# Kernel optimization log

Measured on AMD Instinct MI355X. Metric: run time of the kernel, lower is better.

Reference implementation:

```python
import jax, jax.numpy as jnp
import numpy as np

T, D, H, E, K = 8192, 2048, 7168, 8, 2


def setup_inputs() -> dict:
    key = jax.random.key(0)
    ks = jax.random.split(key, 5)
    s = 0.02
    return {
        "x": jax.random.normal(ks[0], (T, D), jnp.float32),
        "gate_w": jax.random.normal(ks[1], (E, D), jnp.float32) * s,
        "w1": jax.random.normal(ks[2], (E, H, D), jnp.float32) * s,
        "w2": jax.random.normal(ks[3], (E, H, D), jnp.float32) * s,
        "w3": jax.random.normal(ks[4], (E, H, D), jnp.float32) * s,
    }


def reference(x, gate_w, w1, w2, w3):
    # gate logits [T, E]
    logits = x @ gate_w.T
    vals, idx = jax.lax.top_k(logits, K)                      # [T, K]
    w = jax.nn.softmax(vals.astype(jnp.float32), axis=-1).astype(x.dtype)
    # per-token routing weight for each expert (0 if not selected) [T, E]
    tok = jnp.arange(x.shape[0])
    expert_w = jnp.zeros((x.shape[0], E), x.dtype).at[tok[:, None], idx].add(w)

    # scan over experts: dense SwiGLU per expert, weighted accumulate
    def body(acc, ws):
        w1e, w2e, w3e, we = ws  # [H,D],[H,D],[H,D],[T]
        y = (jax.nn.silu(x @ w1e.T) * (x @ w3e.T)) @ w2e      # [T, D]
        return acc + we[:, None] * y, None

    res, _ = jax.lax.scan(body, jnp.zeros_like(x), (w1, w2, w3, expert_w.T))
    return res
```

## Files before the change

kernel.cpp:

```cpp
#include <hip/hip_runtime.h>

#define TT   8192
#define DDIM 2048
#define HDIM 7168
#define NEXP 8
#define MT   32
#define NT1  (HDIM / 128)
#define NT2  (DDIM / 256)
#define NTILE_MAX 72

typedef __attribute__((ext_vector_type(8))) short bf16x8;
typedef __attribute__((ext_vector_type(8))) short short8v;
typedef __attribute__((ext_vector_type(4))) short short4v;
typedef __attribute__((ext_vector_type(4))) float f32x4;

__device__ __forceinline__ unsigned short f2bf(float f) {
  unsigned int u = __builtin_bit_cast(unsigned int, f);
  u += 0x7fffu + ((u >> 16) & 1u);
  return (unsigned short)(u >> 16);
}

__device__ __forceinline__ float bf2f(unsigned short h) {
  unsigned int u = ((unsigned int)h) << 16;
  return __builtin_bit_cast(float, u);
}

__device__ __forceinline__ void gload_lds16(const void* gp, void* lp) {
  __builtin_amdgcn_global_load_lds((__attribute__((address_space(1))) void*)gp,
                                   (__attribute__((address_space(3))) void*)lp,
                                   16, 0, 0);
}

__device__ __forceinline__ void mfma16(f32x4& c, bf16x8 a, bf16x8 b) {
  c = __builtin_amdgcn_mfma_f32_16x16x32_bf16(a, b, c, 0, 0, 0);
}

__device__ __forceinline__ void wg_barrier() {
  asm volatile("" ::: "memory");
  __builtin_amdgcn_s_barrier();
  asm volatile("" ::: "memory");
}

#define PH(H, BA, BB, RDB, STG, SRCP, SOFF, VM)                              \
  do {                                                                       \
    if (RDB) {                                                               \
      _Pragma("unroll")                                                      \
      for (int n = 0; n < 4; ++n)                                            \
        bfr[n] = *(const bf16x8*)(smem + (BB) + rB + n * 1024);              \
    }                                                                        \
    _Pragma("unroll")                                                        \
    for (int m = 0; m < 4; ++m)                                              \
      af[m] = *(const bf16x8*)(smem + (BA) + rA + ((H) + m) * 1024);         \
    if ((STG) >= 0) {                                                        \
      gload_lds16(SRCP[0] + (SOFF), smem + (STG) + wid * 2048);              \
      gload_lds16(SRCP[1] + (SOFF), smem + (STG) + wid * 2048 + 1024);       \
    }                                                                        \
    wg_barrier();                                                            \
    __builtin_amdgcn_s_setprio(1);                                           \
    _Pragma("unroll")                                                        \
    for (int n = 0; n < 4; ++n) {                                            \
      _Pragma("unroll")                                                      \
      for (int m = 0; m < 4; ++m)                                            \
        mfma16(acc[(H) + m][n], af[m], bfr[n]);                              \
    }                                                                        \
    __builtin_amdgcn_s_setprio(0);                                           \
    if ((VM) == 6) asm volatile("s_waitcnt vmcnt(6)" ::: "memory");          \
    if ((VM) == 0) asm volatile("s_waitcnt vmcnt(0)" ::: "memory");          \
    wg_barrier();                                                            \
  } while (0)

#define ITER_FULL(kb)                                                        \
  PH(0, 0,     32768,  1, 81920,  asrc, (kb) + 192, -1);                     \
  PH(4, 0,     32768,  0, 32768,  bsrc, (kb) + 256, -1);                     \
  PH(0, 16384, 49152,  1, 0,      asrc, (kb) + 256, -1);                     \
  PH(4, 16384, 49152,  0, 49152,  bsrc, (kb) + 320,  6);                     \
  PH(0, 65536, 98304,  1, 16384,  asrc, (kb) + 320, -1);                     \
  PH(4, 65536, 98304,  0, 98304,  bsrc, (kb) + 384, -1);                     \
  PH(0, 81920, 114688, 1, 65536,  asrc, (kb) + 384, -1);                     \
  PH(4, 81920, 114688, 0, 114688, bsrc, (kb) + 448,  6);

#define ITER_LAST(kb)                                                        \
  PH(0, 0,     32768,  1, 81920,  asrc, (kb) + 192, -1);                     \
  PH(4, 0,     32768,  0, -1,     asrc, 0,          -1);                     \
  PH(0, 16384, 49152,  1, -1,     asrc, 0,          -1);                     \
  PH(4, 16384, 49152,  0, -1,     asrc, 0,           0);                     \
  PH(0, 65536, 98304,  1, -1,     asrc, 0,          -1);                     \
  PH(4, 65536, 98304,  0, -1,     asrc, 0,          -1);                     \
  PH(0, 81920, 114688, 1, -1,     asrc, 0,          -1);                     \
  PH(4, 81920, 114688, 0, -1,     asrc, 0,          -1);

#define PROLOGUE()                                                           \
  do {                                                                       \
    gload_lds16(asrc[0] + 0,   smem + 0      + wid * 2048);                  \
    gload_lds16(asrc[1] + 0,   smem + 0      + wid * 2048 + 1024);           \
    gload_lds16(bsrc[0] + 0,   smem + 32768  + wid * 2048);                  \
    gload_lds16(bsrc[1] + 0,   smem + 32768  + wid * 2048 + 1024);           \
    gload_lds16(asrc[0] + 64,  smem + 16384  + wid * 2048);                  \
    gload_lds16(asrc[1] + 64,  smem + 16384  + wid * 2048 + 1024);           \
    gload_lds16(bsrc[0] + 64,  smem + 49152  + wid * 2048);                  \
    gload_lds16(bsrc[1] + 64,  smem + 49152  + wid * 2048 + 1024);           \
    gload_lds16(bsrc[0] + 128, smem + 98304  + wid * 2048);                  \
    gload_lds16(bsrc[1] + 128, smem + 98304  + wid * 2048 + 1024);           \
    gload_lds16(asrc[0] + 128, smem + 65536  + wid * 2048);                  \
    gload_lds16(asrc[1] + 128, smem + 65536  + wid * 2048 + 1024);           \
    gload_lds16(bsrc[0] + 192, smem + 114688 + wid * 2048);                  \
    gload_lds16(bsrc[1] + 192, smem + 114688 + wid * 2048 + 1024);           \
    asm volatile("s_waitcnt vmcnt(6)" ::: "memory");                         \
    wg_barrier();                                                            \
  } while (0)

__global__ __launch_bounds__(256) void cvt_bf16_kernel(const float* __restrict__ src,
                                                       unsigned short* __restrict__ dst,
                                                       long n8) {
  long i = (long)blockIdx.x * 256 + threadIdx.x;
  long stride = (long)gridDim.x * 256;
  for (; i < n8; i += stride) {
    float4 a = ((const float4*)src)[i * 2];
    float4 b = ((const float4*)src)[i * 2 + 1];
    short8v s;
    s[0] = (short)f2bf(a.x); s[1] = (short)f2bf(a.y);
    s[2] = (short)f2bf(a.z); s[3] = (short)f2bf(a.w);
    s[4] = (short)f2bf(b.x); s[5] = (short)f2bf(b.y);
    s[6] = (short)f2bf(b.z); s[7] = (short)f2bf(b.w);
    ((short8v*)dst)[i] = s;
  }
}

__global__ __launch_bounds__(256) void gate_kernel(const float* __restrict__ x,
                                                   const float* __restrict__ gw,
                                                   int* __restrict__ route_e,
                                                   float* __restrict__ route_w,
                                                   int* __restrict__ counts) {
  int t = blockIdx.x;
  int tid = threadIdx.x;
  const float* xr = x + (size_t)t * DDIM;
  float p[NEXP];
#pragma unroll
  for (int e = 0; e < NEXP; ++e) p[e] = 0.f;
#pragma unroll
  for (int c = 0; c < DDIM / (256 * 4); ++c) {
    int d = (c * 256 + tid) * 4;
    float4 xv = *(const float4*)(xr + d);
#pragma unroll
    for (int e = 0; e < NEXP; ++e) {
      float4 wv = *(const float4*)(gw + (size_t)e * DDIM + d);
      p[e] += xv.x * wv.x + xv.y * wv.y + xv.z * wv.z + xv.w * wv.w;
    }
  }
  __shared__ float red[NEXP][4];
  int lane = tid & 63, wid = tid >> 6;
#pragma unroll
  for (int e = 0; e < NEXP; ++e) {
    float v = p[e];
    for (int o = 32; o > 0; o >>= 1) v += __shfl_down(v, o);
    if (lane == 0) red[e][wid] = v;
  }
  __syncthreads();
  if (tid == 0) {
    float lg[NEXP];
#pragma unroll
    for (int e = 0; e < NEXP; ++e) lg[e] = red[e][0] + red[e][1] + red[e][2] + red[e][3];
    int i0 = 0;
#pragma unroll
    for (int e = 1; e < NEXP; ++e) if (lg[e] > lg[i0]) i0 = e;
    int i1 = -1;
#pragma unroll
    for (int e = 0; e < NEXP; ++e) {
      if (e == i0) continue;
      if (i1 < 0 || lg[e] > lg[i1]) i1 = e;
    }
    float w0 = 1.f / (1.f + __expf(lg[i1] - lg[i0]));
    float w1 = 1.f - w0;
    route_e[t * 2 + 0] = i0;  route_e[t * 2 + 1] = i1;
    route_w[t * 2 + 0] = w0;  route_w[t * 2 + 1] = w1;
    atomicAdd(&counts[i0], 1);
    atomicAdd(&counts[i1], 1);
  }
}

__global__ void scan_kernel(const int* __restrict__ counts, int* __restrict__ offsets,
                            int* __restrict__ cursor, int* __restrict__ tmap) {
  if (threadIdx.x == 0 && blockIdx.x == 0) {
    int o = 0, idx = 0;
    for (int e = 0; e < NEXP; ++e) {
      offsets[e] = o; cursor[e] = o;
      int c = counts[e]; o += c;
      for (int t = 0; t * 256 < c && idx < NTILE_MAX; ++t) tmap[1 + idx++] = (e << 16) | t;
    }
    tmap[0] = idx;
  }
}

__global__ __launch_bounds__(256) void scatter_kernel(const int* __restrict__ route_e,
                                                      const float* __restrict__ route_w,
                                                      int* __restrict__ cursor,
                                                      int* __restrict__ tok_list,
                                                      float* __restrict__ tok_w,
                                                      int* __restrict__ slot_of) {
  int t = blockIdx.x * 256 + threadIdx.x;
  if (t >= TT) return;
#pragma unroll
  for (int s = 0; s < 2; ++s) {
    int e = route_e[t * 2 + s];
    int p = atomicAdd(&cursor[e], 1);
    tok_list[p] = t;
    tok_w[p] = route_w[t * 2 + s];
    slot_of[t * 2 + s] = p;
  }
}

__global__ __launch_bounds__(256) void transpose_w2_kernel(const float* __restrict__ w2,
                                                           unsigned short* __restrict__ w2t,
                                                           int expert_fixed) {
  int e = expert_fixed >= 0 ? expert_fixed : (int)blockIdx.z;
  const float* src = w2 + (size_t)e * HDIM * DDIM;
  unsigned short* dst = w2t + (expert_fixed >= 0 ? (size_t)0 : (size_t)e * DDIM * HDIM);
  int h0 = blockIdx.x * 64, d0 = blockIdx.y * 64;
  __shared__ __align__(8) unsigned short tile[64 * 66];
  int tid = threadIdx.x;
  int hr = tid >> 2;
#pragma unroll
  for (int j = 0; j < 4; ++j) {
    int f4 = (tid & 3) + j * 4;
    float4 v = *(const float4*)(src + (size_t)(h0 + hr) * DDIM + d0 + f4 * 4);
    unsigned int lo = (unsigned int)f2bf(v.x) | ((unsigned int)f2bf(v.y) << 16);
    unsigned int hi = (unsigned int)f2bf(v.z) | ((unsigned int)f2bf(v.w) << 16);
    char* bp = (char*)tile + hr * 132 + f4 * 8;
    *(unsigned int*)bp = lo;
    *(unsigned int*)(bp + 4) = hi;
  }
  __syncthreads();
  int dr = tid >> 2;
  int hbase = (tid & 3) * 16;
  unsigned short vals[16];
#pragma unroll
  for (int i = 0; i < 16; ++i)
    vals[i] = *(unsigned short*)((char*)tile + (hbase + i) * 132 + dr * 2);
  unsigned short* op = dst + (size_t)(d0 + dr) * HDIM + h0 + hbase;
  short8v s0, s1;
#pragma unroll
  for (int i = 0; i < 8; ++i) { s0[i] = (short)vals[i]; s1[i] = (short)vals[i + 8]; }
  *(short8v*)(op) = s0;
  *(short8v*)(op + 8) = s1;
}

__global__ __launch_bounds__(256) void reduce_kernel(const unsigned short* __restrict__ ybuf,
                                                     const int* __restrict__ slot_of,
                                                     const float* __restrict__ route_w,
                                                     float* __restrict__ out) {
  int t = blockIdx.x;
  int d = threadIdx.x * 8;
  int s0 = slot_of[t * 2 + 0], s1 = slot_of[t * 2 + 1];
  float w0 = route_w[t * 2 + 0], w1 = route_w[t * 2 + 1];
  bf16x8 y0 = *(const bf16x8*)(ybuf + (size_t)s0 * DDIM + d);
  bf16x8 y1 = *(const bf16x8*)(ybuf + (size_t)s1 * DDIM + d);
  float4 o0, o1;
  o0.x = w0 * bf2f((unsigned short)y0[0]) + w1 * bf2f((unsigned short)y1[0]);
  o0.y = w0 * bf2f((unsigned short)y0[1]) + w1 * bf2f((unsigned short)y1[1]);
  o0.z = w0 * bf2f((unsigned short)y0[2]) + w1 * bf2f((unsigned short)y1[2]);
  o0.w = w0 * bf2f((unsigned short)y0[3]) + w1 * bf2f((unsigned short)y1[3]);
  o1.x = w0 * bf2f((unsigned short)y0[4]) + w1 * bf2f((unsigned short)y1[4]);
  o1.y = w0 * bf2f((unsigned short)y0[5]) + w1 * bf2f((unsigned short)y1[5]);
  o1.z = w0 * bf2f((unsigned short)y0[6]) + w1 * bf2f((unsigned short)y1[6]);
  o1.w = w0 * bf2f((unsigned short)y0[7]) + w1 * bf2f((unsigned short)y1[7]);
  float* op = out + (size_t)t * DDIM + d;
  *(float4*)op = o0;
  *(float4*)(op + 4) = o1;
}

__global__ __launch_bounds__(512, 2) void gemm1_kernel(
    const unsigned short* __restrict__ xbf, const unsigned short* __restrict__ w1b,
    const unsigned short* __restrict__ w3b, const int* __restrict__ tok_list,
    const int* __restrict__ counts, const int* __restrict__ offsets,
    const int* __restrict__ tmap,
    unsigned short* __restrict__ g, int expert_fixed) {
  __shared__ __align__(16) char smem[133120];
  constexpr int NI = DDIM / 128;

  int nwg = gridDim.x;
  int orig = blockIdx.x;
  int wg = (orig & 7) * (nwg >> 3) + (orig >> 3);
  int e, mbase, nt;
  if (expert_fixed >= 0) {
    e = expert_fixed;
    mbase = (wg & (MT - 1)) * 256;
    nt = (wg >> 5) % NT1;
  } else {
    int tl = wg % NTILE_MAX;
    nt = wg / NTILE_MAX;
    if (tl >= tmap[0]) return;
    int pk = tmap[1 + tl];
    e = pk >> 16;
    mbase = (pk & 0xffff) * 256;
  }
  int cnt = counts[e];
  if (mbase >= cnt) return;
  int off = offsets[e];
  int gshift = expert_fixed >= 0 ? 0 : off;
  int rows = cnt - mbase; if (rows > 256) rows = 256;

  const unsigned short* w1e = expert_fixed >= 0 ? w1b : w1b + (size_t)e * HDIM * DDIM;
  const unsigned short* w3e = expert_fixed >= 0 ? w3b : w3b + (size_t)e * HDIM * DDIM;

  int tid = threadIdx.x, lane = tid & 63, wid = tid >> 6;
  int wr = wid >> 2, wc = wid & 3;

  int r16 = lane >> 2;
  int csrc = (lane & 3) ^ ((lane >> 3) & 3);
  const char* asrc[2]; const char* bsrc[2];
#pragma unroll
  for (int j = 0; j < 2; ++j) {
    int r = wid * 32 + j * 16 + r16;
    int m = mbase + r; if (m > cnt - 1) m = cnt - 1;
    int tok = tok_list[off + m];
    asrc[j] = (const char*)xbf + (size_t)tok * (DDIM * 2) + csrc * 16;
    const char* base = (r < 128)
        ? (const char*)w1e + (size_t)(nt * 128 + r) * (DDIM * 2)
        : (const char*)w3e + (size_t)(nt * 128 + r - 128) * (DDIM * 2);
    bsrc[j] = base + csrc * 16;
  }
  int rA = (wr * 128 + (lane & 15)) * 64 + (((lane >> 4) ^ ((lane >> 1) & 3)) * 16);
  int rB = (wc * 64  + (lane & 15)) * 64 + (((lane >> 4) ^ ((lane >> 1) & 3)) * 16);

  f32x4 zv = {0.f, 0.f, 0.f, 0.f};
  f32x4 acc[8][4];
#pragma unroll
  for (int m = 0; m < 8; ++m)
#pragma unroll
    for (int n = 0; n < 4; ++n) acc[m][n] = zv;
  bf16x8 af[4], bfr[4];

  PROLOGUE();
#pragma unroll 1
  for (int i = 0; i < NI - 1; ++i) {
    size_t kb = (size_t)i * 256;
    ITER_FULL(kb);
  }
  {
    size_t kb = (size_t)(NI - 1) * 256;
    ITER_LAST(kb);
  }

  float* hb = (float*)smem;
  if (wc < 2) {
#pragma unroll
    for (int m = 0; m < 8; ++m)
#pragma unroll
      for (int q = 0; q < 4; ++q) {
        int row = wr * 128 + m * 16 + (lane >> 4) * 4 + q;
        int col = wc * 64 + (lane & 15);
#pragma unroll
        for (int n = 0; n < 4; ++n)
          hb[row * 130 + col + n * 16] = acc[m][n][q];
      }
  }
  asm volatile("s_waitcnt lgkmcnt(0)" ::: "memory");
  wg_barrier();
  if (wc >= 2) {
#pragma unroll
    for (int m = 0; m < 8; ++m)
#pragma unroll
      for (int q = 0; q < 4; ++q) {
        int row = wr * 128 + m * 16 + (lane >> 4) * 4 + q;
        if (row >= rows) continue;
        size_t grow = (size_t)(mbase + row + gshift);
        int colbase = (wc - 2) * 64 + (lane & 15);
        unsigned short* gp = g + grow * HDIM + nt * 128 + colbase;
#pragma unroll
        for (int n = 0; n < 4; ++n) {
          float h1 = hb[row * 130 + colbase + n * 16];
          float h3 = acc[m][n][q];
          float gv = (h1 / (1.f + __expf(-h1))) * h3;
          gp[n * 16] = f2bf(gv);
        }
      }
  }
}

__global__ __launch_bounds__(512, 2) void gemm2_kernel(
    const unsigned short* __restrict__ g, const unsigned short* __restrict__ w2t,
    const int* __restrict__ tok_list, const float* __restrict__ tok_w,
    const int* __restrict__ counts, const int* __restrict__ offsets,
    const int* __restrict__ tmap,
    unsigned short* __restrict__ ybuf, float* __restrict__ out, int expert_fixed) {
  __shared__ __align__(16) char smem[131072];
  constexpr int NI = HDIM / 128;

  int nwg = gridDim.x;
  int orig = blockIdx.x;
  int wg = (orig & 7) * (nwg >> 3) + (orig >> 3);
  int e, mbase, nt;
  if (expert_fixed >= 0) {
    e = expert_fixed;
    nt = wg % NT2;
    mbase = (wg / NT2) * 256;
  } else {
    int tl = wg / NT2;
    nt = wg % NT2;
    if (tl >= tmap[0]) return;
    int pk = tmap[1 + tl];
    e = pk >> 16;
    mbase = (pk & 0xffff) * 256;
  }
  int cnt = counts[e];
  if (mbase >= cnt) return;
  int off = offsets[e];
  int gshift = expert_fixed >= 0 ? 0 : off;
  int nbase = nt * 256;
  int rows = cnt - mbase; if (rows > 256) rows = 256;
  const unsigned short* w2te = w2t + (expert_fixed >= 0 ? (size_t)0 : (size_t)e * DDIM * HDIM);

  int tid = threadIdx.x, lane = tid & 63, wid = tid >> 6;
  int wr = wid >> 2, wc = wid & 3;

  int r16 = lane >> 2;
  int csrc = (lane & 3) ^ ((lane >> 3) & 3);
  const char* asrc[2]; const char* bsrc[2];
#pragma unroll
  for (int j = 0; j < 2; ++j) {
    int r = wid * 32 + j * 16 + r16;
    int m = mbase + r; if (m > cnt - 1) m = cnt - 1;
    asrc[j] = (const char*)g + (size_t)(m + gshift) * (HDIM * 2) + csrc * 16;
    bsrc[j] = (const char*)w2te + (size_t)(nbase + r) * (HDIM * 2) + csrc * 16;
  }
  int rA = (wr * 128 + (lane & 15)) * 64 + (((lane >> 4) ^ ((lane >> 1) & 3)) * 16);
  int rB = (wc * 64  + (lane & 15)) * 64 + (((lane >> 4) ^ ((lane >> 1) & 3)) * 16);

  f32x4 zv = {0.f, 0.f, 0.f, 0.f};
  f32x4 acc[8][4];
#pragma unroll
  for (int m = 0; m < 8; ++m)
#pragma unroll
    for (int n = 0; n < 4; ++n) acc[m][n] = zv;
  bf16x8 af[4], bfr[4];

  PROLOGUE();
#pragma unroll 1
  for (int i = 0; i < NI - 1; ++i) {
    size_t kb = (size_t)i * 256;
    ITER_FULL(kb);
  }
  {
    size_t kb = (size_t)(NI - 1) * 256;
    ITER_LAST(kb);
  }

  if (ybuf) {
#pragma unroll
    for (int m = 0; m < 8; ++m)
#pragma unroll
      for (int q = 0; q < 4; ++q) {
        int row = wr * 128 + m * 16 + (lane >> 4) * 4 + q;
        if (row >= rows) continue;
        size_t slot = (size_t)(off + mbase + row);
        unsigned short* yp = ybuf + slot * DDIM + nbase + wc * 64 + (lane & 15);
#pragma unroll
        for (int n = 0; n < 4; ++n)
          yp[n * 16] = f2bf(acc[m][n][q]);
      }
  } else {
#pragma unroll
    for (int m = 0; m < 8; ++m)
#pragma unroll
      for (int q = 0; q < 4; ++q) {
        int row = wr * 128 + m * 16 + (lane >> 4) * 4 + q;
        if (row >= rows) continue;
        int mi = mbase + row;
        int tok = tok_list[off + mi];
        float wt = tok_w[off + mi];
        float* op = out + (size_t)tok * DDIM + nbase + wc * 64 + (lane & 15);
#pragma unroll
        for (int n = 0; n < 4; ++n)
          atomicAdd(op + n * 16, acc[m][n][q] * wt);
      }
  }
}

extern "C" void kernel_launch(void* const* d_in, const int* in_sizes, int n_in,
                              void* d_out, int out_size, void* d_ws, size_t ws_size,
                              hipStream_t stream) {
  const float* x      = (const float*)d_in[0];
  const float* gate_w = (const float*)d_in[1];
  const float* w1     = (const float*)d_in[2];
  const float* w2     = (const float*)d_in[3];
  const float* w3     = (const float*)d_in[4];
  float* out = (float*)d_out;
  char* ws = (char*)d_ws;

  size_t o = 0;
  int* counts  = (int*)(ws + o);
  int* offsets = counts + 8;
  int* cursor  = counts + 16;
  int* tmap    = counts + 24;
  o += 1024;
  int*   route_e = (int*)(ws + o);   o += (size_t)TT * 2 * 4;
  float* route_w = (float*)(ws + o); o += (size_t)TT * 2 * 4;
  int*   tok_list = (int*)(ws + o);  o += (size_t)TT * 2 * 4;
  float* tok_w = (float*)(ws + o);   o += (size_t)TT * 2 * 4;
  int*   slot_of = (int*)(ws + o);   o += (size_t)TT * 2 * 4;
  unsigned short* xbf = (unsigned short*)(ws + o); o += (size_t)TT * DDIM * 2;
  size_t fixed = o;

  const size_t WSZ = (size_t)HDIM * DDIM;
  const size_t wbf_full = (size_t)NEXP * WSZ * 2;
  const size_t gfull = (size_t)TT * 2 * HDIM * 2;

  hipMemsetAsync(counts, 0, 8 * sizeof(int), stream);
  cvt_bf16_kernel<<<4096, 256, 0, stream>>>(x, xbf, (long)TT * DDIM / 8);
  gate_kernel<<<TT, 256, 0, stream>>>(x, gate_w, route_e, route_w, counts);
  scan_kernel<<<1, 64, 0, stream>>>(counts, offsets, cursor, tmap);
  scatter_kernel<<<(TT + 255) / 256, 256, 0, stream>>>(route_e, route_w, cursor,
                                                       tok_list, tok_w, slot_of);

  if (ws_size >= fixed + 3 * wbf_full + gfull) {
    unsigned short* w1b = (unsigned short*)(ws + fixed);
    unsigned short* w3b = w1b + NEXP * WSZ;
    unsigned short* w2t = w3b + NEXP * WSZ;
    unsigned short* gbuf = w2t + NEXP * WSZ;
    unsigned short* ybuf = w1b;
    cvt_bf16_kernel<<<8192, 256, 0, stream>>>(w1, w1b, (long)(NEXP * WSZ / 8));
    cvt_bf16_kernel<<<8192, 256, 0, stream>>>(w3, w3b, (long)(NEXP * WSZ / 8));
    transpose_w2_kernel<<<dim3(HDIM / 64, DDIM / 64, NEXP), 256, 0, stream>>>(w2, w2t, -1);
    gemm1_kernel<<<NTILE_MAX * NT1, 512, 0, stream>>>(
        xbf, w1b, w3b, tok_list, counts, offsets, tmap, gbuf, -1);
    gemm2_kernel<<<NTILE_MAX * NT2, 512, 0, stream>>>(
        gbuf, w2t, tok_list, tok_w, counts, offsets, tmap, ybuf, out, -1);
    reduce_kernel<<<TT, 256, 0, stream>>>(ybuf, slot_of, route_w, out);
  } else {
    unsigned short* w1b = (unsigned short*)(ws + fixed);
    unsigned short* w3b = w1b + WSZ;
    unsigned short* w2t = w3b + WSZ;
    unsigned short* gbuf = w2t + WSZ;
    hipMemsetAsync(out, 0, (size_t)TT * DDIM * sizeof(float), stream);
    for (int e = 0; e < NEXP; ++e) {
      cvt_bf16_kernel<<<4096, 256, 0, stream>>>(w1 + (size_t)e * WSZ, w1b, (long)(WSZ / 8));
      cvt_bf16_kernel<<<4096, 256, 0, stream>>>(w3 + (size_t)e * WSZ, w3b, (long)(WSZ / 8));
      transpose_w2_kernel<<<dim3(HDIM / 64, DDIM / 64, 1), 256, 0, stream>>>(w2, w2t, e);
      gemm1_kernel<<<MT * NT1, 512, 0, stream>>>(
          xbf, w1b, w3b, tok_list, counts, offsets, tmap, gbuf, e);
      gemm2_kernel<<<MT * NT2, 512, 0, stream>>>(
          gbuf, w2t, tok_list, tok_w, counts, offsets, tmap, (unsigned short*)0, out, e);
    }
  }
}
```

Measured before the change: 2.254 ms.

## Double-buffer B fragments and prefetch next B tile from LDS during MFMA

Replaces the compiler-generated LDS reads with inline ds_read_b128 and keeps two B-fragment register sets. The next phase's B fragments are read while the current phase's MFMAs run, with explicit lgkmcnt waits and sched_barriers added. The aim is to hide LDS read latency behind matrix math in both GEMM kernels. In exchange it uses more VGPRs, and the manual waitcnt bookkeeping could race if the counts are wrong.

```diff
diff --git a/kernel.cpp b/kernel.cpp
--- a/kernel.cpp
+++ b/kernel.cpp
@@ -13,6 +13,7 @@
 typedef __attribute__((ext_vector_type(8))) short short8v;
 typedef __attribute__((ext_vector_type(4))) short short4v;
 typedef __attribute__((ext_vector_type(4))) float f32x4;
+typedef const __attribute__((address_space(3))) char* lds_ptr;
 
 __device__ __forceinline__ unsigned short f2bf(float f) {
   unsigned int u = __builtin_bit_cast(unsigned int, f);
@@ -35,59 +36,69 @@
   c = __builtin_amdgcn_mfma_f32_16x16x32_bf16(a, b, c, 0, 0, 0);
 }
 
+__device__ __forceinline__ bf16x8 ds_read128(lds_ptr p) {
+  bf16x8 r;
+  asm volatile("ds_read_b128 %0, %1" : "=&v"(r) : "v"(p));
+  return r;
+}
+
 __device__ __forceinline__ void wg_barrier() {
   asm volatile("" ::: "memory");
   __builtin_amdgcn_s_barrier();
   asm volatile("" ::: "memory");
 }
 
-#define PH(H, BA, BB, RDB, STG, SRCP, SOFF, VM)                              \
+#define PH(H, BA, BFC, NBB, BFN, STG, SRCP, SOFF, LGK, VM)                   \
   do {                                                                       \
-    if (RDB) {                                                               \
+    _Pragma("unroll")                                                        \
+    for (int m = 0; m < 4; ++m)                                              \
+      af[m] = ds_read128(lds3 + (BA) + rA + ((H) + m) * 1024);               \
+    if ((NBB) >= 0) {                                                        \
       _Pragma("unroll")                                                      \
       for (int n = 0; n < 4; ++n)                                            \
-        bfr[n] = *(const bf16x8*)(smem + (BB) + rB + n * 1024);              \
+        BFN[n] = ds_read128(lds3 + (NBB) + rB + n * 1024);                   \
     }                                                                        \
-    _Pragma("unroll")                                                        \
-    for (int m = 0; m < 4; ++m)                                              \
-      af[m] = *(const bf16x8*)(smem + (BA) + rA + ((H) + m) * 1024);         \
     if ((STG) >= 0) {                                                        \
       gload_lds16(SRCP[0] + (SOFF), smem + (STG) + wid * 2048);              \
       gload_lds16(SRCP[1] + (SOFF), smem + (STG) + wid * 2048 + 1024);       \
     }                                                                        \
     wg_barrier();                                                            \
+    if ((LGK) == 4) asm volatile("s_waitcnt lgkmcnt(4)" ::: "memory");       \
+    else            asm volatile("s_waitcnt lgkmcnt(0)" ::: "memory");       \
+    __builtin_amdgcn_sched_barrier(0);                                       \
     __builtin_amdgcn_s_setprio(1);                                           \
     _Pragma("unroll")                                                        \
     for (int n = 0; n < 4; ++n) {                                            \
       _Pragma("unroll")                                                      \
       for (int m = 0; m < 4; ++m)                                            \
-        mfma16(acc[(H) + m][n], af[m], bfr[n]);                              \
+        mfma16(acc[(H) + m][n], af[m], BFC[n]);                              \
     }                                                                        \
     __builtin_amdgcn_s_setprio(0);                                           \
+    __builtin_amdgcn_sched_barrier(0);                                       \
     if ((VM) == 6) asm volatile("s_waitcnt vmcnt(6)" ::: "memory");          \
     if ((VM) == 0) asm volatile("s_waitcnt vmcnt(0)" ::: "memory");          \
     wg_barrier();                                                            \
   } while (0)
 
 #define ITER_FULL(kb)                                                        \
-  PH(0, 0,     32768,  1, 81920,  asrc, (kb) + 192, -1);                     \
-  PH(4, 0,     32768,  0, 32768,  bsrc, (kb) + 256, -1);                     \
-  PH(0, 16384, 49152,  1, 0,      asrc, (kb) + 256, -1);                     \
-  PH(4, 16384, 49152,  0, 49152,  bsrc, (kb) + 320,  6);                     \
-  PH(0, 65536, 98304,  1, 16384,  asrc, (kb) + 320, -1);                     \
-  PH(4, 65536, 98304,  0, 98304,  bsrc, (kb) + 384, -1);                     \
-  PH(0, 81920, 114688, 1, 65536,  asrc, (kb) + 384, -1);                     \
-  PH(4, 81920, 114688, 0, 114688, bsrc, (kb) + 448,  6);
+  PH(0, 0,     bfA, -1,     bfB, 81920,  asrc, (kb) + 192, 0, -1);           \
+  PH(4, 0,     bfA, 49152,  bfB, 32768,  bsrc, (kb) + 256, 4,  6);           \
+  PH(0, 16384, bfB, -1,     bfA, 0,      asrc, (kb) + 256, 0, -1);           \
+  PH(4, 16384, bfB, 98304,  bfA, 49152,  bsrc, (kb) + 320, 4,  6);           \
+  PH(0, 65536, bfA, -1,     bfB, 16384,  asrc, (kb) + 320, 0, -1);           \
+  PH(4, 65536, bfA, 114688, bfB, 98304,  bsrc, (kb) + 384, 4,  6);           \
+  PH(0, 81920, bfB, -1,     bfA, 65536,  asrc, (kb) + 384, 0, -1);           \
+  PH(4, 81920, bfB, 32768,  bfA, 114688, bsrc, (kb) + 448, 4,  6);
 
 #define ITER_LAST(kb)                                                        \
-  PH(0, 0,     32768,  1, 81920,  asrc, (kb) + 192, -1);                     \
-  PH(4, 0,     32768,  0, -1,     asrc, 0,          -1);                     \
-  PH(0, 16384, 49152,  1, -1,     asrc, 0,          -1);                     \
-  PH(4, 16384, 49152,  0, -1,     asrc, 0,           0);                     \
-  PH(0, 65536, 98304,  1, -1,     asrc, 0,          -1);                     \
-  PH(4, 65536, 98304,  0, -1,     asrc, 0,          -1);                     \
-  PH(0, 81920, 114688, 1, -1,     asrc, 0,          -1);                     \
-  PH(4, 81920, 114688, 0, -1,     asrc, 0,          -1);
+  PH(0, 0,     bfA, -1,     bfB, 81920, asrc, (kb) + 192, 0, -1);            \
+  PH(4, 0,     bfA, 49152,  bfB, -1,    asrc, 0,          4,  6);            \
+  PH(0, 16384, bfB, -1,     bfA, -1,    asrc, 0,          0, -1);            \
+  PH(4, 16384, bfB, 98304,  bfA, -1,    asrc, 0,          4,  0);            \
+  PH(0, 65536, bfA, -1,     bfB, -1,    asrc, 0,          0, -1);            \
+  PH(4, 65536, bfA, 114688, bfB, -1,    asrc, 0,          4, -1);            \
+  PH(0, 81920, bfB, -1,     bfA, -1,    asrc, 0,          0, -1);            \
+  PH(4, 81920, bfB, -1,     bfA, -1,    asrc, 0,          0, -1);
 
 #define PROLOGUE()                                                           \
   do {                                                                       \
@@ -107,6 +118,9 @@
     gload_lds16(bsrc[1] + 192, smem + 114688 + wid * 2048 + 1024);           \
     asm volatile("s_waitcnt vmcnt(6)" ::: "memory");                         \
     wg_barrier();                                                            \
+    _Pragma("unroll")                                                        \
+    for (int n = 0; n < 4; ++n)                                              \
+      bfA[n] = ds_read128(lds3 + 32768 + rB + n * 1024);                     \
   } while (0)
 
 __global__ __launch_bounds__(256) void cvt_bf16_kernel(const float* __restrict__ src,
@@ -304,6 +318,7 @@
 
   int tid = threadIdx.x, lane = tid & 63, wid = tid >> 6;
   int wr = wid >> 2, wc = wid & 3;
+  lds_ptr lds3 = (lds_ptr)smem;
 
   int r16 = lane >> 2;
   int csrc = (lane & 3) ^ ((lane >> 3) & 3);
@@ -328,7 +343,7 @@
   for (int m = 0; m < 8; ++m)
 #pragma unroll
     for (int n = 0; n < 4; ++n) acc[m][n] = zv;
-  bf16x8 af[4], bfr[4];
+  bf16x8 af[4], bfA[4], bfB[4];
 
   PROLOGUE();
 #pragma unroll 1
@@ -340,6 +355,8 @@
     size_t kb = (size_t)(NI - 1) * 256;
     ITER_LAST(kb);
   }
+  asm volatile("s_waitcnt lgkmcnt(0)" ::: "memory");
+  __builtin_amdgcn_sched_barrier(0);
 
   float* hb = (float*)smem;
   if (wc < 2) {
@@ -412,6 +429,7 @@
 
   int tid = threadIdx.x, lane = tid & 63, wid = tid >> 6;
   int wr = wid >> 2, wc = wid & 3;
+  lds_ptr lds3 = (lds_ptr)smem;
 
   int r16 = lane >> 2;
   int csrc = (lane & 3) ^ ((lane >> 3) & 3);
@@ -432,7 +450,7 @@
   for (int m = 0; m < 8; ++m)
 #pragma unroll
     for (int n = 0; n < 4; ++n) acc[m][n] = zv;
-  bf16x8 af[4], bfr[4];
+  bf16x8 af[4], bfA[4], bfB[4];
 
   PROLOGUE();
 #pragma unroll 1
@@ -444,6 +462,8 @@
     size_t kb = (size_t)(NI - 1) * 256;
     ITER_LAST(kb);
   }
+  asm volatile("s_waitcnt lgkmcnt(0)" ::: "memory");
+  __builtin_amdgcn_sched_barrier(0);
 
   if (ybuf) {
 #pragma unroll
```

Result: slower. 2.352 ms (+4.4%).

## Split gemm2 K dimension in two and sum partials in reduce

Applied to the files above, without the earlier changes.

Splits the down-projection GEMM's K (hidden) dimension into two halves handled by separate workgroups, doubling the grid to fill more CUs. Each half writes bf16 partials to a separate ybuf region, and the reduce kernel sums both partials before applying routing weights. This adds extra partial write/read traffic and an extra bf16 rounding of partials in exchange for better occupancy on gemm2, which had only 8 N-tiles per M-tile. The ybuf second half sits at offset TT*2*DDIM inside the w1b region, which must be large enough.

```diff
diff --git a/kernel.cpp b/kernel.cpp
--- a/kernel.cpp
+++ b/kernel.cpp
@@ -7,6 +7,7 @@
 #define MT   32
 #define NT1  (HDIM / 128)
 #define NT2  (DDIM / 256)
+#define KSPL 2
 #define NTILE_MAX 72
 
 typedef __attribute__((ext_vector_type(8))) short bf16x8;
@@ -248,24 +249,22 @@
                                                      const int* __restrict__ slot_of,
                                                      const float* __restrict__ route_w,
                                                      float* __restrict__ out) {
+  const size_t YSZ = (size_t)TT * 2 * DDIM;
   int t = blockIdx.x;
   int d = threadIdx.x * 8;
   int s0 = slot_of[t * 2 + 0], s1 = slot_of[t * 2 + 1];
   float w0 = route_w[t * 2 + 0], w1 = route_w[t * 2 + 1];
-  bf16x8 y0 = *(const bf16x8*)(ybuf + (size_t)s0 * DDIM + d);
-  bf16x8 y1 = *(const bf16x8*)(ybuf + (size_t)s1 * DDIM + d);
-  float4 o0, o1;
-  o0.x = w0 * bf2f((unsigned short)y0[0]) + w1 * bf2f((unsigned short)y1[0]);
-  o0.y = w0 * bf2f((unsigned short)y0[1]) + w1 * bf2f((unsigned short)y1[1]);
-  o0.z = w0 * bf2f((unsigned short)y0[2]) + w1 * bf2f((unsigned short)y1[2]);
-  o0.w = w0 * bf2f((unsigned short)y0[3]) + w1 * bf2f((unsigned short)y1[3]);
-  o1.x = w0 * bf2f((unsigned short)y0[4]) + w1 * bf2f((unsigned short)y1[4]);
-  o1.y = w0 * bf2f((unsigned short)y0[5]) + w1 * bf2f((unsigned short)y1[5]);
-  o1.z = w0 * bf2f((unsigned short)y0[6]) + w1 * bf2f((unsigned short)y1[6]);
-  o1.w = w0 * bf2f((unsigned short)y0[7]) + w1 * bf2f((unsigned short)y1[7]);
+  bf16x8 y0a = *(const bf16x8*)(ybuf + (size_t)s0 * DDIM + d);
+  bf16x8 y0b = *(const bf16x8*)(ybuf + YSZ + (size_t)s0 * DDIM + d);
+  bf16x8 y1a = *(const bf16x8*)(ybuf + (size_t)s1 * DDIM + d);
+  bf16x8 y1b = *(const bf16x8*)(ybuf + YSZ + (size_t)s1 * DDIM + d);
   float* op = out + (size_t)t * DDIM + d;
-  *(float4*)op = o0;
-  *(float4*)(op + 4) = o1;
+#pragma unroll
+  for (int j = 0; j < 8; ++j) {
+    float v0 = bf2f((unsigned short)y0a[j]) + bf2f((unsigned short)y0b[j]);
+    float v1 = bf2f((unsigned short)y1a[j]) + bf2f((unsigned short)y1b[j]);
+    op[j] = w0 * v0 + w1 * v1;
+  }
 }
 
 __global__ __launch_bounds__(512, 2) void gemm1_kernel(
@@ -384,19 +383,21 @@
     const int* __restrict__ tmap,
     unsigned short* __restrict__ ybuf, float* __restrict__ out, int expert_fixed) {
   __shared__ __align__(16) char smem[131072];
-  constexpr int NI = HDIM / 128;
+  constexpr int NI = HDIM / 128 / KSPL;
 
   int nwg = gridDim.x;
   int orig = blockIdx.x;
   int wg = (orig & 7) * (nwg >> 3) + (orig >> 3);
-  int e, mbase, nt;
+  int e, mbase, nt, ks;
   if (expert_fixed >= 0) {
     e = expert_fixed;
     nt = wg % NT2;
-    mbase = (wg / NT2) * 256;
+    ks = (wg / NT2) % KSPL;
+    mbase = (wg / (NT2 * KSPL)) * 256;
   } else {
-    int tl = wg / NT2;
     nt = wg % NT2;
+    ks = (wg / NT2) % KSPL;
+    int tl = wg / (NT2 * KSPL);
     if (tl >= tmap[0]) return;
     int pk = tmap[1 + tl];
     e = pk >> 16;
@@ -409,6 +410,7 @@
   int nbase = nt * 256;
   int rows = cnt - mbase; if (rows > 256) rows = 256;
   const unsigned short* w2te = w2t + (expert_fixed >= 0 ? (size_t)0 : (size_t)e * DDIM * HDIM);
+  size_t koff = (size_t)ks * (NI * 256);
 
   int tid = threadIdx.x, lane = tid & 63, wid = tid >> 6;
   int wr = wid >> 2, wc = wid & 3;
@@ -420,8 +422,8 @@
   for (int j = 0; j < 2; ++j) {
     int r = wid * 32 + j * 16 + r16;
     int m = mbase + r; if (m > cnt - 1) m = cnt - 1;
-    asrc[j] = (const char*)g + (size_t)(m + gshift) * (HDIM * 2) + csrc * 16;
-    bsrc[j] = (const char*)w2te + (size_t)(nbase + r) * (HDIM * 2) + csrc * 16;
+    asrc[j] = (const char*)g + (size_t)(m + gshift) * (HDIM * 2) + csrc * 16 + koff;
+    bsrc[j] = (const char*)w2te + (size_t)(nbase + r) * (HDIM * 2) + csrc * 16 + koff;
   }
   int rA = (wr * 128 + (lane & 15)) * 64 + (((lane >> 4) ^ ((lane >> 1) & 3)) * 16);
   int rB = (wc * 64  + (lane & 15)) * 64 + (((lane >> 4) ^ ((lane >> 1) & 3)) * 16);
@@ -446,6 +448,7 @@
   }
 
   if (ybuf) {
+    unsigned short* yb = ybuf + (size_t)ks * ((size_t)TT * 2 * DDIM);
 #pragma unroll
     for (int m = 0; m < 8; ++m)
 #pragma unroll
@@ -453,7 +456,7 @@
         int row = wr * 128 + m * 16 + (lane >> 4) * 4 + q;
         if (row >= rows) continue;
         size_t slot = (size_t)(off + mbase + row);
-        unsigned short* yp = ybuf + slot * DDIM + nbase + wc * 64 + (lane & 15);
+        unsigned short* yp = yb + slot * DDIM + nbase + wc * 64 + (lane & 15);
 #pragma unroll
         for (int n = 0; n < 4; ++n)
           yp[n * 16] = f2bf(acc[m][n][q]);
@@ -523,7 +526,7 @@
     transpose_w2_kernel<<<dim3(HDIM / 64, DDIM / 64, NEXP), 256, 0, stream>>>(w2, w2t, -1);
     gemm1_kernel<<<NTILE_MAX * NT1, 512, 0, stream>>>(
         xbf, w1b, w3b, tok_list, counts, offsets, tmap, gbuf, -1);
-    gemm2_kernel<<<NTILE_MAX * NT2, 512, 0, stream>>>(
+    gemm2_kernel<<<NTILE_MAX * NT2 * KSPL, 512, 0, stream>>>(
         gbuf, w2t, tok_list, tok_w, counts, offsets, tmap, ybuf, out, -1);
     reduce_kernel<<<TT, 256, 0, stream>>>(ybuf, slot_of, route_w, out);
   } else {
@@ -538,7 +541,7 @@
       transpose_w2_kernel<<<dim3(HDIM / 64, DDIM / 64, 1), 256, 0, stream>>>(w2, w2t, e);
       gemm1_kernel<<<MT * NT1, 512, 0, stream>>>(
           xbf, w1b, w3b, tok_list, counts, offsets, tmap, gbuf, e);
-      gemm2_kernel<<<MT * NT2, 512, 0, stream>>>(
+      gemm2_kernel<<<MT * NT2 * KSPL, 512, 0, stream>>>(
           gbuf, w2t, tok_list, tok_w, counts, offsets, tmap, (unsigned short*)0, out, e);
     }
   }
```

New measurement: 2.230 ms. No clear change (-1.0%).
